# Kernel tuning notes

Measured on AMD Instinct MI355X. Metric: run time of the kernel, lower is better.

Reference implementation:

```python
import jax, jax.numpy as jnp
import numpy as np

N_NODES = 50000
D = 256
N_EDGES = 262144
N_LAYER = 3
EPS = 1e-5


def setup_inputs() -> dict:
    key = jax.random.key(0)
    ks = jax.random.split(key, 8)
    x = jax.random.normal(ks[0], (N_NODES, D), dtype=jnp.float32)
    jg_edge_index = jax.random.randint(ks[1], (2, N_EDGES), 0, N_NODES, dtype=jnp.int64)
    ln_w = jnp.ones((D,), dtype=jnp.float32)
    # torch Linear weight is [out, in]; stack per-layer weights [L, D, D]
    Ws = jax.random.normal(ks[2], (N_LAYER, D, D), dtype=jnp.float32) * (1.0 / np.sqrt(D))
    gammas = jnp.ones((N_LAYER, D), dtype=jnp.float32)
    betas = jnp.zeros((N_LAYER, D), dtype=jnp.float32)
    W_out = jax.random.normal(ks[3], (1, D), dtype=jnp.float32) * (1.0 / np.sqrt(D))
    return {"x": x, "jg_edge_index": jg_edge_index, "ln_w": ln_w,
            "Ws": Ws, "gammas": gammas, "betas": betas, "W_out": W_out}


def reference(x, jg_edge_index, ln_w, Ws, gammas, betas, W_out):
    src, dst = jg_edge_index[0], jg_edge_index[1]
    # edge features: gather + add -> [E, D]
    h = x[src, :] + x[dst, :]
    # LayerNorm over feature dim, weight only (bias=False), eps=1e-5
    mu = jnp.mean(h, axis=-1, keepdims=True)
    var = jnp.mean(jnp.square(h - mu), axis=-1, keepdims=True)
    h = (h - mu) * jax.lax.rsqrt(var + EPS) * ln_w
    # projection blocks: Linear (no bias) -> BatchNorm1d (training stats) -> ReLU
    for i in range(N_LAYER):
        h = h @ Ws[i].T  # [E, D]
        bmu = jnp.mean(h, axis=0)                      # batch mean over edges
        bvar = jnp.mean(jnp.square(h - bmu), axis=0)   # biased batch var
        h = (h - bmu) * jax.lax.rsqrt(bvar + EPS) * gammas[i] + betas[i]
        h = jax.nn.relu(h)
    logits = (h @ W_out.T).squeeze(-1)  # [E]
    return logits
```

## Files before the change

kernel.cpp:

```cpp
#include <hip/hip_runtime.h>
#include <hip/hip_bf16.h>

#define NEDGE 262144
#define DIM 256
#define NLAYER 3
#define EPSV 1e-5f

#define GBM 512
#define RC 64
#define NCH (GBM / RC)
#define GEMM_GRID (NEDGE / GBM)

typedef __attribute__((ext_vector_type(8))) short bf16x8_t;
typedef __attribute__((ext_vector_type(4))) float f32x4_t;

__device__ __forceinline__ float bf2f(short s) {
  unsigned u = ((unsigned)(unsigned short)s) << 16;
  return __builtin_bit_cast(float, u);
}
__device__ __forceinline__ short f2bf(float f) {
  __hip_bfloat16 h = __float2bfloat16(f);
  return __builtin_bit_cast(short, h);
}

extern "C" __global__ void __launch_bounds__(256)
k_cvt(const float* __restrict__ src, short* __restrict__ dst, int n) {
  int i = blockIdx.x * 256 + threadIdx.x;
  if (i < n) dst[i] = f2bf(src[i]);
}

extern "C" __global__ void __launch_bounds__(256)
k_edge_ln(const float* __restrict__ x, const int* __restrict__ ei,
          const float* __restrict__ lnw, short* __restrict__ h0) {
  const int e = (blockIdx.x << 2) + (threadIdx.x >> 6);
  const int lane = threadIdx.x & 63;
  const int src = ei[e];
  const int dst = ei[NEDGE + e];
  const float4 a = *(const float4*)(x + (size_t)src * DIM + lane * 4);
  const float4 b = *(const float4*)(x + (size_t)dst * DIM + lane * 4);
  const float v0 = a.x + b.x, v1 = a.y + b.y, v2 = a.z + b.z, v3 = a.w + b.w;
  float s = v0 + v1 + v2 + v3;
  float ss = v0 * v0 + v1 * v1 + v2 * v2 + v3 * v3;
#pragma unroll
  for (int off = 32; off >= 1; off >>= 1) {
    s += __shfl_xor(s, off);
    ss += __shfl_xor(ss, off);
  }
  const float mu = s * (1.0f / DIM);
  const float var = ss * (1.0f / DIM) - mu * mu;
  const float sc = rsqrtf(var + EPSV);
  const float4 w = *(const float4*)(lnw + lane * 4);
  ushort4 o;
  o.x = (unsigned short)f2bf((v0 - mu) * sc * w.x);
  o.y = (unsigned short)f2bf((v1 - mu) * sc * w.y);
  o.z = (unsigned short)f2bf((v2 - mu) * sc * w.z);
  o.w = (unsigned short)f2bf((v3 - mu) * sc * w.w);
  *(ushort4*)(h0 + (size_t)e * DIM + lane * 4) = o;
}

template <int HASBN>
__global__ void __launch_bounds__(512, 2)
k_gemm_p(const short* __restrict__ A, const short* __restrict__ W,
         short* __restrict__ C, float* __restrict__ psum, float* __restrict__ psq,
         const float* __restrict__ bsc, const float* __restrict__ bsh) {
  __shared__ short As[2][RC * DIM];
  const int tid = threadIdx.x;
  const int w = tid >> 6;
  const int lane = tid & 63;
  const int rl = lane & 15;
  const int kh = lane >> 4;
  const int row0 = blockIdx.x * GBM;
  const int colbase = w * 32;

  bf16x8_t wf[2][8];
#pragma unroll
  for (int n = 0; n < 2; ++n)
#pragma unroll
    for (int ks = 0; ks < 8; ++ks)
      wf[n][ks] = *(const bf16x8_t*)(W + (size_t)(colbase + n * 16 + rl) * DIM + ks * 32 + kh * 8);

  const int cst = tid & 31;
  float sc0[8], sh0[8];
  if (HASBN) {
#pragma unroll
    for (int j = 0; j < 8; ++j) {
      sc0[j] = bsc[cst * 8 + j];
      sh0[j] = bsh[cst * 8 + j];
    }
  }

  float st_s0 = 0.f, st_s1 = 0.f, st_q0 = 0.f, st_q1 = 0.f;

  auto stage_lds = [&](int t, int b) {
#pragma unroll
    for (int i = 0; i < 4; ++i) {
      const int r_lo = w * 8 + i * 2;
      const int row = r_lo + (lane >> 5);
      const int c = lane & 31;
      const short* gp = A + (size_t)(row0 + t * RC + row) * DIM + ((c ^ (row & 7)) << 3);
      short* lp = &As[b][r_lo * DIM];
      __builtin_amdgcn_global_load_lds(
          (const __attribute__((address_space(1))) unsigned int*)gp,
          (__attribute__((address_space(3))) unsigned int*)lp, 16, 0, 0);
    }
  };

  auto ldreg = [&](int t, bf16x8_t* r) {
#pragma unroll
    for (int i = 0; i < 4; ++i) {
      const int row = (tid + i * 512) >> 5;
      r[i] = *(const bf16x8_t*)(A + (size_t)(row0 + t * RC + row) * DIM + cst * 8);
    }
  };
  auto xform_write = [&](int b, bf16x8_t* r) {
#pragma unroll
    for (int i = 0; i < 4; ++i) {
      const int row = (tid + i * 512) >> 5;
      bf16x8_t v = r[i];
      bf16x8_t o;
#pragma unroll
      for (int j = 0; j < 8; ++j)
        o[j] = f2bf(fmaxf(fmaf(bf2f(v[j]), sc0[j], sh0[j]), 0.0f));
      *(bf16x8_t*)(&As[b][row * DIM + ((cst ^ (row & 7)) << 3)]) = o;
    }
  };

  auto compute = [&](int t, int b) {
    const f32x4_t zero = {0.f, 0.f, 0.f, 0.f};
    f32x4_t acc[4][2];
#pragma unroll
    for (int m = 0; m < 4; ++m) {
      acc[m][0] = zero;
      acc[m][1] = zero;
    }
    const short* base = As[b];
#pragma unroll
    for (int ks = 0; ks < 8; ++ks) {
      bf16x8_t af[4];
#pragma unroll
      for (int m = 0; m < 4; ++m) {
        const int row = m * 16 + rl;
        const int c = ks * 4 + kh;
        af[m] = *(const bf16x8_t*)(base + row * DIM + ((c ^ (row & 7)) << 3));
      }
#pragma unroll
      for (int m = 0; m < 4; ++m) {
        acc[m][0] = __builtin_amdgcn_mfma_f32_16x16x32_bf16(af[m], wf[0][ks], acc[m][0], 0, 0, 0);
        acc[m][1] = __builtin_amdgcn_mfma_f32_16x16x32_bf16(af[m], wf[1][ks], acc[m][1], 0, 0, 0);
      }
    }
    const int rquad = kh << 2;
#pragma unroll
    for (int n = 0; n < 2; ++n) {
      const int col = colbase + n * 16 + rl;
      float s = 0.f, q = 0.f;
#pragma unroll
      for (int m = 0; m < 4; ++m) {
        const size_t rb = (size_t)(row0 + t * RC + m * 16 + rquad) * DIM + col;
#pragma unroll
        for (int r = 0; r < 4; ++r) {
          const float f = acc[m][n][r];
          C[rb + (size_t)r * DIM] = f2bf(f);
          s += f;
          q = fmaf(f, f, q);
        }
      }
      if (n == 0) { st_s0 += s; st_q0 += q; }
      else        { st_s1 += s; st_q1 += q; }
    }
  };

  if (HASBN == 0) {
    stage_lds(0, 0);
    for (int t = 0; t < NCH; ++t) {
      __syncthreads();
      if (t + 1 < NCH) stage_lds(t + 1, (t + 1) & 1);
      compute(t, t & 1);
    }
  } else {
    bf16x8_t ra[4], rb[4];
    ldreg(0, ra);
    xform_write(0, ra);
    ldreg(1, rb);
    __syncthreads();
    for (int t = 0; t < NCH; ++t) {
      if (t + 2 < NCH) ldreg(t + 2, ra);
      compute(t, t & 1);
      if (t + 1 < NCH) xform_write((t + 1) & 1, rb);
      __syncthreads();
#pragma unroll
      for (int i = 0; i < 4; ++i) { bf16x8_t tmp = ra[i]; ra[i] = rb[i]; rb[i] = tmp; }
    }
  }

  {
    float s = st_s0, q = st_q0;
    s += __shfl_xor(s, 16); s += __shfl_xor(s, 32);
    q += __shfl_xor(q, 16); q += __shfl_xor(q, 32);
    if (lane < 16) {
      psum[(size_t)blockIdx.x * DIM + colbase + rl] = s;
      psq [(size_t)blockIdx.x * DIM + colbase + rl] = q;
    }
  }
  {
    float s = st_s1, q = st_q1;
    s += __shfl_xor(s, 16); s += __shfl_xor(s, 32);
    q += __shfl_xor(q, 16); q += __shfl_xor(q, 32);
    if (lane < 16) {
      psum[(size_t)blockIdx.x * DIM + colbase + 16 + rl] = s;
      psq [(size_t)blockIdx.x * DIM + colbase + 16 + rl] = q;
    }
  }
}

extern "C" __global__ void __launch_bounds__(64)
k_stats(const float* __restrict__ psum, const float* __restrict__ psq,
        const float* __restrict__ gamma, const float* __restrict__ beta,
        float* __restrict__ sc, float* __restrict__ sh, int nblk) {
  const int c = blockIdx.x;
  const int lane = threadIdx.x;
  float s = 0.0f, q = 0.0f;
  for (int b = lane; b < nblk; b += 64) {
    s += psum[(size_t)b * DIM + c];
    q += psq[(size_t)b * DIM + c];
  }
#pragma unroll
  for (int off = 32; off >= 1; off >>= 1) {
    s += __shfl_xor(s, off);
    q += __shfl_xor(q, off);
  }
  if (lane == 0) {
    const float inv = 1.0f / NEDGE;
    const float mu = s * inv;
    const float var = q * inv - mu * mu;
    const float scale = rsqrtf(var + EPSV) * gamma[c];
    sc[c] = scale;
    sh[c] = beta[c] - mu * scale;
  }
}

extern "C" __global__ void __launch_bounds__(256)
k_head(const short* __restrict__ h3, const float* __restrict__ sc,
       const float* __restrict__ sh, const float* __restrict__ wout,
       float* __restrict__ out) {
  const int e = (blockIdx.x << 2) + (threadIdx.x >> 6);
  const int lane = threadIdx.x & 63;
  const ushort4 v = *(const ushort4*)(h3 + (size_t)e * DIM + lane * 4);
  const int c = lane * 4;
  float acc = fmaxf(bf2f((short)v.x) * sc[c + 0] + sh[c + 0], 0.0f) * wout[c + 0];
  acc += fmaxf(bf2f((short)v.y) * sc[c + 1] + sh[c + 1], 0.0f) * wout[c + 1];
  acc += fmaxf(bf2f((short)v.z) * sc[c + 2] + sh[c + 2], 0.0f) * wout[c + 2];
  acc += fmaxf(bf2f((short)v.w) * sc[c + 3] + sh[c + 3], 0.0f) * wout[c + 3];
#pragma unroll
  for (int off = 32; off >= 1; off >>= 1) acc += __shfl_xor(acc, off);
  if (lane == 0) out[e] = acc;
}

extern "C" void kernel_launch(void* const* d_in, const int* in_sizes, int n_in,
                              void* d_out, int out_size, void* d_ws, size_t ws_size,
                              hipStream_t stream) {
  const float* x = (const float*)d_in[0];
  const int* ei = (const int*)d_in[1];
  const float* lnw = (const float*)d_in[2];
  const float* Ws = (const float*)d_in[3];
  const float* gammas = (const float*)d_in[4];
  const float* betas = (const float*)d_in[5];
  const float* wout = (const float*)d_in[6];
  float* out = (float*)d_out;

  char* ws = (char*)d_ws;
  const size_t HBYTES = (size_t)NEDGE * DIM * 2;
  short* h = (short*)ws;
  short* Wb = (short*)(ws + HBYTES);
  char* p = ws + HBYTES + (size_t)NLAYER * DIM * DIM * 2;
  float* psum = (float*)p;
  float* psq = psum + (size_t)GEMM_GRID * DIM;
  float* bnsc = psq + (size_t)GEMM_GRID * DIM;
  float* bnsh = bnsc + NLAYER * DIM;

  k_cvt<<<(NLAYER * DIM * DIM + 255) / 256, 256, 0, stream>>>(Ws, Wb, NLAYER * DIM * DIM);
  k_edge_ln<<<NEDGE / 4, 256, 0, stream>>>(x, ei, lnw, h);

  for (int l = 0; l < NLAYER; ++l) {
    const float* sc = (l == 0) ? nullptr : bnsc + (size_t)(l - 1) * DIM;
    const float* sh = (l == 0) ? nullptr : bnsh + (size_t)(l - 1) * DIM;
    if (l == 0)
      k_gemm_p<0><<<GEMM_GRID, 512, 0, stream>>>(h, Wb + (size_t)l * DIM * DIM, h,
                                                 psum, psq, sc, sh);
    else
      k_gemm_p<1><<<GEMM_GRID, 512, 0, stream>>>(h, Wb + (size_t)l * DIM * DIM, h,
                                                 psum, psq, sc, sh);
    k_stats<<<DIM, 64, 0, stream>>>(psum, psq, gammas + (size_t)l * DIM,
                                    betas + (size_t)l * DIM,
                                    bnsc + (size_t)l * DIM, bnsh + (size_t)l * DIM,
                                    GEMM_GRID);
  }
  k_head<<<NEDGE / 4, 256, 0, stream>>>(h, bnsc + (size_t)(NLAYER - 1) * DIM,
                                        bnsh + (size_t)(NLAYER - 1) * DIM, wout, out);
}
```

Before: 310.1 us.

## Fuse edge gather and LayerNorm into first GEMM; widen head kernel vectors

The separate gather+LayerNorm kernel is removed. The first projection GEMM now gathers x rows by edge index, computes LayerNorm in registers and writes bf16 tiles straight to LDS, with the next chunk's gather prefetched during compute. This avoids writing and then re-reading the normalized edge features through HBM. The head kernel now handles 8 edges per block using 8-wide bf16 loads. The trade-off is that the fused GEMM holds many float4 gather registers, which may lower occupancy and expose gather latency.

```diff
diff --git a/kernel.cpp b/kernel.cpp
--- a/kernel.cpp
+++ b/kernel.cpp
@@ -29,40 +29,157 @@
   if (i < n) dst[i] = f2bf(src[i]);
 }
 
-extern "C" __global__ void __launch_bounds__(256)
-k_edge_ln(const float* __restrict__ x, const int* __restrict__ ei,
-          const float* __restrict__ lnw, short* __restrict__ h0) {
-  const int e = (blockIdx.x << 2) + (threadIdx.x >> 6);
-  const int lane = threadIdx.x & 63;
-  const int src = ei[e];
-  const int dst = ei[NEDGE + e];
-  const float4 a = *(const float4*)(x + (size_t)src * DIM + lane * 4);
-  const float4 b = *(const float4*)(x + (size_t)dst * DIM + lane * 4);
-  const float v0 = a.x + b.x, v1 = a.y + b.y, v2 = a.z + b.z, v3 = a.w + b.w;
-  float s = v0 + v1 + v2 + v3;
-  float ss = v0 * v0 + v1 * v1 + v2 * v2 + v3 * v3;
-#pragma unroll
-  for (int off = 32; off >= 1; off >>= 1) {
-    s += __shfl_xor(s, off);
-    ss += __shfl_xor(ss, off);
-  }
-  const float mu = s * (1.0f / DIM);
-  const float var = ss * (1.0f / DIM) - mu * mu;
-  const float sc = rsqrtf(var + EPSV);
-  const float4 w = *(const float4*)(lnw + lane * 4);
-  ushort4 o;
-  o.x = (unsigned short)f2bf((v0 - mu) * sc * w.x);
-  o.y = (unsigned short)f2bf((v1 - mu) * sc * w.y);
-  o.z = (unsigned short)f2bf((v2 - mu) * sc * w.z);
-  o.w = (unsigned short)f2bf((v3 - mu) * sc * w.w);
-  *(ushort4*)(h0 + (size_t)e * DIM + lane * 4) = o;
-}
-
-template <int HASBN>
-__global__ void __launch_bounds__(512, 2)
-k_gemm_p(const short* __restrict__ A, const short* __restrict__ W,
-         short* __restrict__ C, float* __restrict__ psum, float* __restrict__ psq,
-         const float* __restrict__ bsc, const float* __restrict__ bsh) {
+extern "C" __global__ void __launch_bounds__(512)
+k_gemm1f(const float* __restrict__ x, const int* __restrict__ ei,
+         const float* __restrict__ lnw, const short* __restrict__ W,
+         short* __restrict__ C, float* __restrict__ psum, float* __restrict__ psq) {
+  __shared__ short As[2][RC * DIM];
+  __shared__ int sIdx[GBM], dIdx[GBM];
+  const int tid = threadIdx.x;
+  const int w = tid >> 6;
+  const int lane = tid & 63;
+  const int rl = lane & 15;
+  const int kh = lane >> 4;
+  const int row0 = blockIdx.x * GBM;
+  const int colbase = w * 32;
+  const int cst = tid & 31;
+
+  sIdx[tid] = ei[row0 + tid];
+  dIdx[tid] = ei[NEDGE + row0 + tid];
+
+  bf16x8_t wf[2][8];
+#pragma unroll
+  for (int n = 0; n < 2; ++n)
+#pragma unroll
+    for (int ks = 0; ks < 8; ++ks)
+      wf[n][ks] = *(const bf16x8_t*)(W + (size_t)(colbase + n * 16 + rl) * DIM + ks * 32 + kh * 8);
+
+  float lw[8];
+#pragma unroll
+  for (int j = 0; j < 8; ++j) lw[j] = lnw[cst * 8 + j];
+
+  float st_s0 = 0.f, st_s1 = 0.f, st_q0 = 0.f, st_q1 = 0.f;
+  float4 rs0[4], rs1[4], rd0[4], rd1[4];
+
+  auto ldgather = [&](int t) {
+#pragma unroll
+    for (int i = 0; i < 4; ++i) {
+      const int r = (tid >> 5) + 16 * i;
+      const int s = sIdx[t * RC + r];
+      const int d = dIdx[t * RC + r];
+      const float* ps = x + (size_t)s * DIM + cst * 8;
+      const float* pd = x + (size_t)d * DIM + cst * 8;
+      rs0[i] = *(const float4*)ps;
+      rs1[i] = *(const float4*)(ps + 4);
+      rd0[i] = *(const float4*)pd;
+      rd1[i] = *(const float4*)(pd + 4);
+    }
+  };
+
+  auto lnwrite = [&](int b) {
+#pragma unroll
+    for (int i = 0; i < 4; ++i) {
+      const int r = (tid >> 5) + 16 * i;
+      float v[8];
+      v[0] = rs0[i].x + rd0[i].x; v[1] = rs0[i].y + rd0[i].y;
+      v[2] = rs0[i].z + rd0[i].z; v[3] = rs0[i].w + rd0[i].w;
+      v[4] = rs1[i].x + rd1[i].x; v[5] = rs1[i].y + rd1[i].y;
+      v[6] = rs1[i].z + rd1[i].z; v[7] = rs1[i].w + rd1[i].w;
+      float s = 0.f, ss = 0.f;
+#pragma unroll
+      for (int j = 0; j < 8; ++j) { s += v[j]; ss = fmaf(v[j], v[j], ss); }
+#pragma unroll
+      for (int off = 16; off >= 1; off >>= 1) {
+        s += __shfl_xor(s, off);
+        ss += __shfl_xor(ss, off);
+      }
+      const float mu = s * (1.0f / DIM);
+      const float var = ss * (1.0f / DIM) - mu * mu;
+      const float sc = rsqrtf(var + EPSV);
+      bf16x8_t o;
+#pragma unroll
+      for (int j = 0; j < 8; ++j) o[j] = f2bf((v[j] - mu) * sc * lw[j]);
+      *(bf16x8_t*)(&As[b][r * DIM + ((cst ^ (r & 7)) << 3)]) = o;
+    }
+  };
+
+  auto compute = [&](int t, int b) {
+    const f32x4_t zero = {0.f, 0.f, 0.f, 0.f};
+    f32x4_t acc[4][2];
+#pragma unroll
+    for (int m = 0; m < 4; ++m) { acc[m][0] = zero; acc[m][1] = zero; }
+    const short* base = As[b];
+#pragma unroll
+    for (int ks = 0; ks < 8; ++ks) {
+      bf16x8_t af[4];
+#pragma unroll
+      for (int m = 0; m < 4; ++m) {
+        const int row = m * 16 + rl;
+        const int c = ks * 4 + kh;
+        af[m] = *(const bf16x8_t*)(base + row * DIM + ((c ^ (row & 7)) << 3));
+      }
+#pragma unroll
+      for (int m = 0; m < 4; ++m) {
+        acc[m][0] = __builtin_amdgcn_mfma_f32_16x16x32_bf16(af[m], wf[0][ks], acc[m][0], 0, 0, 0);
+        acc[m][1] = __builtin_amdgcn_mfma_f32_16x16x32_bf16(af[m], wf[1][ks], acc[m][1], 0, 0, 0);
+      }
+    }
+    const int rquad = kh << 2;
+#pragma unroll
+    for (int n = 0; n < 2; ++n) {
+      const int col = colbase + n * 16 + rl;
+      float s = 0.f, q = 0.f;
+#pragma unroll
+      for (int m = 0; m < 4; ++m) {
+        const size_t rb = (size_t)(row0 + t * RC + m * 16 + rquad) * DIM + col;
+#pragma unroll
+        for (int r = 0; r < 4; ++r) {
+          const float f = acc[m][n][r];
+          C[rb + (size_t)r * DIM] = f2bf(f);
+          s += f;
+          q = fmaf(f, f, q);
+        }
+      }
+      if (n == 0) { st_s0 += s; st_q0 += q; }
+      else        { st_s1 += s; st_q1 += q; }
+    }
+  };
+
+  __syncthreads();
+  ldgather(0);
+  lnwrite(0);
+  __syncthreads();
+  for (int t = 0; t < NCH; ++t) {
+    if (t + 1 < NCH) ldgather(t + 1);
+    compute(t, t & 1);
+    if (t + 1 < NCH) lnwrite((t + 1) & 1);
+    __syncthreads();
+  }
+
+  {
+    float s = st_s0, q = st_q0;
+    s += __shfl_xor(s, 16); s += __shfl_xor(s, 32);
+    q += __shfl_xor(q, 16); q += __shfl_xor(q, 32);
+    if (lane < 16) {
+      psum[(size_t)blockIdx.x * DIM + colbase + rl] = s;
+      psq [(size_t)blockIdx.x * DIM + colbase + rl] = q;
+    }
+  }
+  {
+    float s = st_s1, q = st_q1;
+    s += __shfl_xor(s, 16); s += __shfl_xor(s, 32);
+    q += __shfl_xor(q, 16); q += __shfl_xor(q, 32);
+    if (lane < 16) {
+      psum[(size_t)blockIdx.x * DIM + colbase + 16 + rl] = s;
+      psq [(size_t)blockIdx.x * DIM + colbase + 16 + rl] = q;
+    }
+  }
+}
+
+extern "C" __global__ void __launch_bounds__(512, 2)
+k_gemm_bn(const short* __restrict__ A, const short* __restrict__ W,
+          short* __restrict__ C, float* __restrict__ psum, float* __restrict__ psq,
+          const float* __restrict__ bsc, const float* __restrict__ bsh) {
   __shared__ short As[2][RC * DIM];
   const int tid = threadIdx.x;
   const int w = tid >> 6;
@@ -81,29 +198,13 @@
 
   const int cst = tid & 31;
   float sc0[8], sh0[8];
-  if (HASBN) {
-#pragma unroll
-    for (int j = 0; j < 8; ++j) {
-      sc0[j] = bsc[cst * 8 + j];
-      sh0[j] = bsh[cst * 8 + j];
-    }
+#pragma unroll
+  for (int j = 0; j < 8; ++j) {
+    sc0[j] = bsc[cst * 8 + j];
+    sh0[j] = bsh[cst * 8 + j];
   }
 
   float st_s0 = 0.f, st_s1 = 0.f, st_q0 = 0.f, st_q1 = 0.f;
-
-  auto stage_lds = [&](int t, int b) {
-#pragma unroll
-    for (int i = 0; i < 4; ++i) {
-      const int r_lo = w * 8 + i * 2;
-      const int row = r_lo + (lane >> 5);
-      const int c = lane & 31;
-      const short* gp = A + (size_t)(row0 + t * RC + row) * DIM + ((c ^ (row & 7)) << 3);
-      short* lp = &As[b][r_lo * DIM];
-      __builtin_amdgcn_global_load_lds(
-          (const __attribute__((address_space(1))) unsigned int*)gp,
-          (__attribute__((address_space(3))) unsigned int*)lp, 16, 0, 0);
-    }
-  };
 
   auto ldreg = [&](int t, bf16x8_t* r) {
 #pragma unroll
@@ -129,10 +230,7 @@
     const f32x4_t zero = {0.f, 0.f, 0.f, 0.f};
     f32x4_t acc[4][2];
 #pragma unroll
-    for (int m = 0; m < 4; ++m) {
-      acc[m][0] = zero;
-      acc[m][1] = zero;
-    }
+    for (int m = 0; m < 4; ++m) { acc[m][0] = zero; acc[m][1] = zero; }
     const short* base = As[b];
 #pragma unroll
     for (int ks = 0; ks < 8; ++ks) {
@@ -170,27 +268,18 @@
     }
   };
 
-  if (HASBN == 0) {
-    stage_lds(0, 0);
-    for (int t = 0; t < NCH; ++t) {
-      __syncthreads();
-      if (t + 1 < NCH) stage_lds(t + 1, (t + 1) & 1);
-      compute(t, t & 1);
-    }
-  } else {
-    bf16x8_t ra[4], rb[4];
-    ldreg(0, ra);
-    xform_write(0, ra);
-    ldreg(1, rb);
+  bf16x8_t ra[4], rb[4];
+  ldreg(0, ra);
+  xform_write(0, ra);
+  ldreg(1, rb);
+  __syncthreads();
+  for (int t = 0; t < NCH; ++t) {
+    if (t + 2 < NCH) ldreg(t + 2, ra);
+    compute(t, t & 1);
+    if (t + 1 < NCH) xform_write((t + 1) & 1, rb);
     __syncthreads();
-    for (int t = 0; t < NCH; ++t) {
-      if (t + 2 < NCH) ldreg(t + 2, ra);
-      compute(t, t & 1);
-      if (t + 1 < NCH) xform_write((t + 1) & 1, rb);
-      __syncthreads();
-#pragma unroll
-      for (int i = 0; i < 4; ++i) { bf16x8_t tmp = ra[i]; ra[i] = rb[i]; rb[i] = tmp; }
-    }
+#pragma unroll
+    for (int i = 0; i < 4; ++i) { bf16x8_t tmp = ra[i]; ra[i] = rb[i]; rb[i] = tmp; }
   }
 
   {
@@ -243,17 +332,17 @@
 k_head(const short* __restrict__ h3, const float* __restrict__ sc,
        const float* __restrict__ sh, const float* __restrict__ wout,
        float* __restrict__ out) {
-  const int e = (blockIdx.x << 2) + (threadIdx.x >> 6);
-  const int lane = threadIdx.x & 63;
-  const ushort4 v = *(const ushort4*)(h3 + (size_t)e * DIM + lane * 4);
-  const int c = lane * 4;
-  float acc = fmaxf(bf2f((short)v.x) * sc[c + 0] + sh[c + 0], 0.0f) * wout[c + 0];
-  acc += fmaxf(bf2f((short)v.y) * sc[c + 1] + sh[c + 1], 0.0f) * wout[c + 1];
-  acc += fmaxf(bf2f((short)v.z) * sc[c + 2] + sh[c + 2], 0.0f) * wout[c + 2];
-  acc += fmaxf(bf2f((short)v.w) * sc[c + 3] + sh[c + 3], 0.0f) * wout[c + 3];
-#pragma unroll
-  for (int off = 32; off >= 1; off >>= 1) acc += __shfl_xor(acc, off);
-  if (lane == 0) out[e] = acc;
+  const int e = (blockIdx.x << 3) + (threadIdx.x >> 5);
+  const int g = threadIdx.x & 31;
+  const int c = g * 8;
+  const bf16x8_t v = *(const bf16x8_t*)(h3 + (size_t)e * DIM + c);
+  float acc = 0.f;
+#pragma unroll
+  for (int j = 0; j < 8; ++j)
+    acc += fmaxf(fmaf(bf2f(v[j]), sc[c + j], sh[c + j]), 0.0f) * wout[c + j];
+#pragma unroll
+  for (int off = 16; off >= 1; off >>= 1) acc += __shfl_xor(acc, off);
+  if (g == 0) out[e] = acc;
 }
 
 extern "C" void kernel_launch(void* const* d_in, const int* in_sizes, int n_in,
@@ -279,22 +368,20 @@
   float* bnsh = bnsc + NLAYER * DIM;
 
   k_cvt<<<(NLAYER * DIM * DIM + 255) / 256, 256, 0, stream>>>(Ws, Wb, NLAYER * DIM * DIM);
-  k_edge_ln<<<NEDGE / 4, 256, 0, stream>>>(x, ei, lnw, h);
-
-  for (int l = 0; l < NLAYER; ++l) {
-    const float* sc = (l == 0) ? nullptr : bnsc + (size_t)(l - 1) * DIM;
-    const float* sh = (l == 0) ? nullptr : bnsh + (size_t)(l - 1) * DIM;
-    if (l == 0)
-      k_gemm_p<0><<<GEMM_GRID, 512, 0, stream>>>(h, Wb + (size_t)l * DIM * DIM, h,
-                                                 psum, psq, sc, sh);
-    else
-      k_gemm_p<1><<<GEMM_GRID, 512, 0, stream>>>(h, Wb + (size_t)l * DIM * DIM, h,
-                                                 psum, psq, sc, sh);
+
+  k_gemm1f<<<GEMM_GRID, 512, 0, stream>>>(x, ei, lnw, Wb, h, psum, psq);
+  k_stats<<<DIM, 64, 0, stream>>>(psum, psq, gammas, betas, bnsc, bnsh, GEMM_GRID);
+
+  for (int l = 1; l < NLAYER; ++l) {
+    k_gemm_bn<<<GEMM_GRID, 512, 0, stream>>>(h, Wb + (size_t)l * DIM * DIM, h,
+                                             psum, psq,
+                                             bnsc + (size_t)(l - 1) * DIM,
+                                             bnsh + (size_t)(l - 1) * DIM);
     k_stats<<<DIM, 64, 0, stream>>>(psum, psq, gammas + (size_t)l * DIM,
                                     betas + (size_t)l * DIM,
                                     bnsc + (size_t)l * DIM, bnsh + (size_t)l * DIM,
                                     GEMM_GRID);
   }
-  k_head<<<NEDGE / 4, 256, 0, stream>>>(h, bnsc + (size_t)(NLAYER - 1) * DIM,
+  k_head<<<NEDGE / 8, 256, 0, stream>>>(h, bnsc + (size_t)(NLAYER - 1) * DIM,
                                         bnsh + (size_t)(NLAYER - 1) * DIM, wout, out);
 }
```

Measured after the change: 267.4 us. -13.8%, faster.
